# Performance work log

Measured on AMD Instinct MI355X. Metric: run time of the kernel, lower is better.

## Reference

```python
import jax, jax.numpy as jnp
import numpy as np

B, SQ, SK, H = 8, 2048, 2048, 256
NH, HD = 4, 64  # num_heads, head_dim


def setup_inputs() -> dict:
    key = jax.random.key(0)
    ks = jax.random.split(key, 9)
    scale = 0.02
    inp = {
        'query': jax.random.normal(ks[0], (B, SQ, H), jnp.float32),
        'key':   jax.random.normal(ks[1], (B, SK, H), jnp.float32),
        'value': jax.random.normal(ks[2], (B, SK, H), jnp.float32),
        'mask':  jax.random.bernoulli(ks[3], 0.9, (B, SQ, SK)),
        'Wq': jax.random.normal(ks[4], (H, H), jnp.float32) * scale,
        'bq': jnp.zeros((H,), jnp.float32),
        'Wk': jax.random.normal(ks[5], (H, H), jnp.float32) * scale,
        'bk': jnp.zeros((H,), jnp.float32),
        'Wv': jax.random.normal(ks[6], (H, H), jnp.float32) * scale,
        'bv': jnp.zeros((H,), jnp.float32),
        'Wo': jax.random.normal(ks[7], (H, H), jnp.float32) * scale,
        'bo': jnp.zeros((H,), jnp.float32),
    }
    return inp


def reference(query, key, value, mask, Wq, bq, Wk, bk, Wv, bv, Wo, bo):
    b = query.shape[0]
    scale = jnp.asarray(HD, query.dtype) ** -0.5
    # torch Linear: x @ W.T + b; reshape to [B, NH, S, HD]
    Q = (query @ Wq.T + bq).reshape(b, -1, NH, HD).transpose(0, 2, 1, 3)
    K = (key   @ Wk.T + bk).reshape(b, -1, NH, HD).transpose(0, 2, 1, 3)
    V = (value @ Wv.T + bv).reshape(b, -1, NH, HD).transpose(0, 2, 1, 3)
    scores = jnp.einsum('bhqd,bhkd->bhqk', Q, K) * scale  # [B,NH,SQ,SK]
    # mask-fixing: rows with no valid key get key 0 unmasked
    mask_sum = mask.sum(axis=-1)  # [B,SQ]
    mask_fixed = mask.at[:, :, 0].set(jnp.where(mask_sum == 0, True, mask[:, :, 0]))
    scores = jnp.where(mask_fixed[:, None, :, :], scores, jnp.asarray(-1e9, scores.dtype))
    attn = jax.nn.softmax(scores, axis=-1)
    attn = jnp.where(jnp.isnan(attn), jnp.zeros_like(attn), attn)  # NaN fix
    out = jnp.einsum('bhqk,bhkd->bhqd', attn, V)
    out = out.transpose(0, 2, 1, 3).reshape(b, -1, H)
    out = out @ Wo.T + bo
    return out, attn
```

## Files before the change

### kernel.cpp

```cpp
#include <hip/hip_runtime.h>
#include <math.h>

#define Bn  8
#define SQn 2048
#define SKn 2048
#define Hn  256
#define NHn 4
#define HDn 64
#define SCALEF 0.125f

typedef __attribute__((ext_vector_type(4))) float f32x4;
typedef __attribute__((ext_vector_type(8))) short short8;

__device__ __forceinline__ unsigned short f2bf(float f) {
  unsigned u = __builtin_bit_cast(unsigned, f);
  u += 0x7fffu + ((u >> 16) & 1u);
  return (unsigned short)(u >> 16);
}

__device__ __forceinline__ short8 load8f(const float* p) {
  float4 v0 = *(const float4*)p;
  float4 v1 = *(const float4*)(p + 4);
  short8 r;
  r[0] = (short)f2bf(v0.x); r[1] = (short)f2bf(v0.y);
  r[2] = (short)f2bf(v0.z); r[3] = (short)f2bf(v0.w);
  r[4] = (short)f2bf(v1.x); r[5] = (short)f2bf(v1.y);
  r[6] = (short)f2bf(v1.z); r[7] = (short)f2bf(v1.w);
  return r;
}

__device__ __forceinline__ f32x4 mfma16(short8 a, short8 b, f32x4 c) {
  return __builtin_amdgcn_mfma_f32_16x16x32_bf16(a, b, c, 0, 0, 0);
}

__global__ void detect_mask(const unsigned* __restrict__ m, int* __restrict__ flag) {
  if (threadIdx.x == 0) {
    int f = 0;
    for (int i = 0; i < 64; ++i)
      if (m[i] > 1u) f = 1;
    flag[0] = f;
  }
}

__global__ __launch_bounds__(256) void proj_kernel(
    const float* __restrict__ X, const float* __restrict__ W,
    const float* __restrict__ bias, unsigned short* __restrict__ Y, int vtrans)
{
  const int m0 = blockIdx.x * 64;
  const int n0 = blockIdx.y * 64;
  const int wv = threadIdx.x >> 6;
  const int l  = threadIdx.x & 63;
  const int lr = l & 15, lg = l >> 4;
  const int mrow = m0 + wv * 16 + lr;

  f32x4 acc[4];
  #pragma unroll
  for (int t = 0; t < 4; ++t) acc[t] = (f32x4){0.f, 0.f, 0.f, 0.f};

  const float* ap = X + (size_t)mrow * Hn + lg * 8;
  for (int k0 = 0; k0 < Hn; k0 += 32) {
    short8 a = load8f(ap + k0);
    #pragma unroll
    for (int t = 0; t < 4; ++t) {
      short8 bb = load8f(W + (size_t)(n0 + t * 16 + lr) * Hn + k0 + lg * 8);
      acc[t] = mfma16(a, bb, acc[t]);
    }
  }

  #pragma unroll
  for (int t = 0; t < 4; ++t) {
    const int n = n0 + t * 16 + lr;
    const float bv = bias[n];
    const int h = n >> 6, d = n & 63;
    if (!vtrans) {
      #pragma unroll
      for (int r = 0; r < 4; ++r) {
        const int m = m0 + wv * 16 + lg * 4 + r;
        const int bb = m >> 11, s = m & 2047;
        size_t idx = (((size_t)bb * NHn + h) * SQn + s) * HDn + d;
        Y[idx] = f2bf(acc[t][r] + bv);
      }
    } else {
      const int m = m0 + wv * 16 + lg * 4;
      const int bb = m >> 11, s = m & 2047;
      ushort4 pk;
      pk.x = f2bf(acc[t][0] + bv); pk.y = f2bf(acc[t][1] + bv);
      pk.z = f2bf(acc[t][2] + bv); pk.w = f2bf(acc[t][3] + bv);
      size_t idx = (((size_t)bb * NHn + h) * HDn + d) * (size_t)SKn + s;
      *(ushort4*)(Y + idx) = pk;
    }
  }
}

template <typename T>
__device__ __forceinline__ void load_mask_bits(const T* __restrict__ mp, size_t rowbase,
                                               int colbase, int lr, unsigned mb[4]) {
  #pragma unroll
  for (int r = 0; r < 4; ++r) {
    const T* rp = mp + rowbase + (size_t)r * SKn + colbase + lr;
    unsigned bits = 0;
    #pragma unroll
    for (int t = 0; t < 16; ++t) bits |= (rp[t * 16] != 0 ? 1u : 0u) << t;
    mb[r] = bits;
  }
}

__global__ __launch_bounds__(512) void attn_kernel(
    const unsigned short* __restrict__ Qb, const unsigned short* __restrict__ Kb,
    const unsigned short* __restrict__ Vt, const void* __restrict__ maskp,
    const int* __restrict__ flagp, float* __restrict__ attn_out,
    unsigned short* __restrict__ Ob)
{
  __shared__ __align__(16) unsigned short Plds[16 * 2048];
  float* red = (float*)Plds;
  float* gv  = (float*)Plds + 128;

  const int q0 = blockIdx.x * 16;
  const int h = blockIdx.y, b = blockIdx.z;
  const int wv = threadIdx.x >> 6;
  const int l = threadIdx.x & 63;
  const int lr = l & 15, lg = l >> 4;
  const int colbase = wv * 256;
  const size_t bh = (size_t)b * NHn + h;

  const unsigned short* Qh = Qb + bh * SQn * HDn;
  const unsigned short* Kh = Kb + bh * SKn * HDn;
  const unsigned short* Vh = Vt + bh * HDn * SKn;

  short8 qa0 = *(const short8*)(Qh + (q0 + lr) * HDn + lg * 8);
  short8 qa1 = *(const short8*)(Qh + (q0 + lr) * HDn + 32 + lg * 8);

  f32x4 sc[16];
  #pragma unroll
  for (int t = 0; t < 16; ++t) {
    const int c0 = colbase + t * 16;
    short8 b0 = *(const short8*)(Kh + (size_t)(c0 + lr) * HDn + lg * 8);
    short8 b1 = *(const short8*)(Kh + (size_t)(c0 + lr) * HDn + 32 + lg * 8);
    f32x4 z = (f32x4){0.f, 0.f, 0.f, 0.f};
    z = mfma16(qa0, b0, z);
    z = mfma16(qa1, b1, z);
    sc[t] = z;
  }

  unsigned mb[4];
  const int q_base = q0 + lg * 4;
  const size_t mrowbase = ((size_t)b * SQn + q_base) * (size_t)SKn;
  if (*flagp) load_mask_bits((const unsigned char*)maskp, mrowbase, colbase, lr, mb);
  else        load_mask_bits((const int*)maskp,           mrowbase, colbase, lr, mb);

  float rmax[4] = {-INFINITY, -INFINITY, -INFINITY, -INFINITY};
  #pragma unroll
  for (int t = 0; t < 16; ++t)
    #pragma unroll
    for (int r = 0; r < 4; ++r)
      if ((mb[r] >> t) & 1) rmax[r] = fmaxf(rmax[r], sc[t][r] * SCALEF);
  #pragma unroll
  for (int m = 1; m < 16; m <<= 1)
    #pragma unroll
    for (int r = 0; r < 4; ++r)
      rmax[r] = fmaxf(rmax[r], __shfl_xor(rmax[r], m));
  if (lr == 0)
    #pragma unroll
    for (int r = 0; r < 4; ++r) red[wv * 16 + lg * 4 + r] = rmax[r];
  __syncthreads();
  if (threadIdx.x < 16) {
    float m = red[threadIdx.x];
    for (int w = 1; w < 8; ++w) m = fmaxf(m, red[w * 16 + threadIdx.x]);
    gv[threadIdx.x] = m;
  }
  __syncthreads();

  float gmax[4], rsum[4] = {0.f, 0.f, 0.f, 0.f};
  #pragma unroll
  for (int r = 0; r < 4; ++r) gmax[r] = gv[lg * 4 + r];

  #pragma unroll
  for (int t = 0; t < 16; ++t) {
    const int col = colbase + t * 16 + lr;
    #pragma unroll
    for (int r = 0; r < 4; ++r) {
      float p;
      if (gmax[r] == -INFINITY) p = (col == 0) ? 1.0f : 0.0f;
      else p = ((mb[r] >> t) & 1) ? __expf(sc[t][r] * SCALEF - gmax[r]) : 0.0f;
      sc[t][r] = p;
      rsum[r] += p;
    }
  }
  #pragma unroll
  for (int m = 1; m < 16; m <<= 1)
    #pragma unroll
    for (int r = 0; r < 4; ++r) rsum[r] += __shfl_xor(rsum[r], m);
  if (lr == 0)
    #pragma unroll
    for (int r = 0; r < 4; ++r) red[wv * 16 + lg * 4 + r] = rsum[r];
  __syncthreads();
  if (threadIdx.x < 16) {
    float s = 0.f;
    for (int w = 0; w < 8; ++w) s += red[w * 16 + threadIdx.x];
    gv[threadIdx.x] = s;
  }
  __syncthreads();
  float rinv[4];
  #pragma unroll
  for (int r = 0; r < 4; ++r) rinv[r] = 1.0f / gv[lg * 4 + r];
  __syncthreads();

  #pragma unroll
  for (int t = 0; t < 16; ++t) {
    const int col = colbase + t * 16 + lr;
    #pragma unroll
    for (int r = 0; r < 4; ++r) {
      const int row = lg * 4 + r;
      float a = sc[t][r] * rinv[r];
      attn_out[(bh * SQn + q0 + row) * (size_t)SKn + col] = a;
      unsigned byteoff = (unsigned)row * 4096u + (unsigned)col * 2u;
      byteoff ^= ((unsigned)(row & 7) << 4);
      *(unsigned short*)((char*)Plds + byteoff) = f2bf(a);
    }
  }
  __syncthreads();

  f32x4 oacc[4];
  #pragma unroll
  for (int dt = 0; dt < 4; ++dt) oacc[dt] = (f32x4){0.f, 0.f, 0.f, 0.f};
  #pragma unroll
  for (int ks = 0; ks < 8; ++ks) {
    const int ck = colbase + ks * 32;
    unsigned aoff = (unsigned)lr * 4096u + (unsigned)(ck + lg * 8) * 2u;
    aoff ^= ((unsigned)(lr & 7) << 4);
    short8 pa = *(const short8*)((char*)Plds + aoff);
    #pragma unroll
    for (int dt = 0; dt < 4; ++dt) {
      short8 vb = *(const short8*)(Vh + (size_t)(dt * 16 + lr) * SKn + ck + lg * 8);
      oacc[dt] = mfma16(pa, vb, oacc[dt]);
    }
  }
  __syncthreads();

  float* Op = (float*)Plds;
  #pragma unroll
  for (int dt = 0; dt < 4; ++dt)
    #pragma unroll
    for (int r = 0; r < 4; ++r)
      Op[(wv * 16 + lg * 4 + r) * 64 + dt * 16 + lr] = oacc[dt][r];
  __syncthreads();
  for (int e = threadIdx.x; e < 1024; e += 512) {
    const int row = e >> 6, d = e & 63;
    float s = 0.f;
    for (int w = 0; w < 8; ++w) s += Op[w * 1024 + row * 64 + d];
    Ob[((size_t)b * SQn + q0 + row) * Hn + h * HDn + d] = f2bf(s);
  }
}

__global__ __launch_bounds__(256) void oproj_kernel(
    const unsigned short* __restrict__ A, const float* __restrict__ W,
    const float* __restrict__ bias, float* __restrict__ out)
{
  const int m0 = blockIdx.x * 64;
  const int n0 = blockIdx.y * 64;
  const int wv = threadIdx.x >> 6;
  const int l  = threadIdx.x & 63;
  const int lr = l & 15, lg = l >> 4;
  const int mrow = m0 + wv * 16 + lr;

  f32x4 acc[4];
  #pragma unroll
  for (int t = 0; t < 4; ++t) acc[t] = (f32x4){0.f, 0.f, 0.f, 0.f};

  for (int k0 = 0; k0 < Hn; k0 += 32) {
    short8 a = *(const short8*)(A + (size_t)mrow * Hn + k0 + lg * 8);
    #pragma unroll
    for (int t = 0; t < 4; ++t) {
      short8 bb = load8f(W + (size_t)(n0 + t * 16 + lr) * Hn + k0 + lg * 8);
      acc[t] = mfma16(a, bb, acc[t]);
    }
  }
  #pragma unroll
  for (int t = 0; t < 4; ++t) {
    const int n = n0 + t * 16 + lr;
    const float bv = bias[n];
    #pragma unroll
    for (int r = 0; r < 4; ++r) {
      const int m = m0 + wv * 16 + lg * 4 + r;
      out[(size_t)m * Hn + n] = acc[t][r] + bv;
    }
  }
}

extern "C" void kernel_launch(void* const* d_in, const int* in_sizes, int n_in,
                              void* d_out, int out_size, void* d_ws, size_t ws_size,
                              hipStream_t stream) {
  const float* query = (const float*)d_in[0];
  const float* key_  = (const float*)d_in[1];
  const float* value = (const float*)d_in[2];
  const void*  mask  = d_in[3];
  const float* Wq = (const float*)d_in[4];
  const float* bq = (const float*)d_in[5];
  const float* Wk = (const float*)d_in[6];
  const float* bk = (const float*)d_in[7];
  const float* Wv = (const float*)d_in[8];
  const float* bv = (const float*)d_in[9];
  const float* Wo = (const float*)d_in[10];
  const float* bo = (const float*)d_in[11];

  float* out  = (float*)d_out;
  float* attn = out + (size_t)Bn * SQn * Hn;

  char* ws = (char*)d_ws;
  int* flag = (int*)ws;
  unsigned short* Qb = (unsigned short*)(ws + 256);
  unsigned short* Kb = Qb + (size_t)Bn * SQn * Hn;
  unsigned short* Vt = Kb + (size_t)Bn * SKn * Hn;
  unsigned short* Ob = Vt + (size_t)Bn * SKn * Hn;

  detect_mask<<<1, 64, 0, stream>>>((const unsigned*)mask, flag);

  dim3 pg(256, 4);
  proj_kernel<<<pg, 256, 0, stream>>>(query, Wq, bq, Qb, 0);
  proj_kernel<<<pg, 256, 0, stream>>>(key_,  Wk, bk, Kb, 0);
  proj_kernel<<<pg, 256, 0, stream>>>(value, Wv, bv, Vt, 1);

  attn_kernel<<<dim3(SQn / 16, NHn, Bn), 512, 0, stream>>>(
      Qb, Kb, Vt, mask, flag, attn, Ob);

  oproj_kernel<<<dim3(256, 4), 256, 0, stream>>>(Ob, Wo, bo, out);
}
```

Measured before the change: 516.0 us.

## Restructure attention to per-wave two-pass online softmax without LDS or block syncs

The 512-thread block that split the key range across 8 waves and reduced through shared memory is replaced by one wave per 16-row query tile. Each wave runs two passes over all keys: an online max/sum pass, then a pass that recomputes scores, writes normalized attention with vectorized stores and feeds bf16 probabilities straight into the PV MFMAs. The mask is read once with wide loads into a bitmask kept in registers, and blocks are remapped with a swizzle. This removes LDS traffic, block barriers and the cross-wave output reduction, at the cost of computing QK^T twice and holding 16 mask words per lane.

```diff
diff --git a/kernel.cpp b/kernel.cpp
--- a/kernel.cpp
+++ b/kernel.cpp
@@ -8,9 +8,13 @@
 #define NHn 4
 #define HDn 64
 #define SCALEF 0.125f
+#define NEGBIG -1e30f
 
 typedef __attribute__((ext_vector_type(4))) float f32x4;
+typedef __attribute__((ext_vector_type(4))) unsigned int u32x4;
 typedef __attribute__((ext_vector_type(8))) short short8;
+typedef unsigned short ushort_t;
+typedef unsigned long long ull_t;
 
 __device__ __forceinline__ unsigned short f2bf(float f) {
   unsigned u = __builtin_bit_cast(unsigned, f);
@@ -92,164 +96,167 @@
   }
 }
 
-template <typename T>
-__device__ __forceinline__ void load_mask_bits(const T* __restrict__ mp, size_t rowbase,
-                                               int colbase, int lr, unsigned mb[4]) {
-  #pragma unroll
-  for (int r = 0; r < 4; ++r) {
-    const T* rp = mp + rowbase + (size_t)r * SKn + colbase + lr;
-    unsigned bits = 0;
-    #pragma unroll
-    for (int t = 0; t < 16; ++t) bits |= (rp[t * 16] != 0 ? 1u : 0u) << t;
-    mb[r] = bits;
-  }
-}
-
-__global__ __launch_bounds__(512) void attn_kernel(
-    const unsigned short* __restrict__ Qb, const unsigned short* __restrict__ Kb,
-    const unsigned short* __restrict__ Vt, const void* __restrict__ maskp,
-    const int* __restrict__ flagp, float* __restrict__ attn_out,
-    unsigned short* __restrict__ Ob)
+template <int BYTEMASK>
+__device__ __forceinline__ void attn_wave(
+    int rt, const ushort_t* __restrict__ Qb, const ushort_t* __restrict__ Kb,
+    const ushort_t* __restrict__ Vt, const void* __restrict__ maskp,
+    float* __restrict__ attn_out, ushort_t* __restrict__ Ob)
 {
-  __shared__ __align__(16) unsigned short Plds[16 * 2048];
-  float* red = (float*)Plds;
-  float* gv  = (float*)Plds + 128;
-
-  const int q0 = blockIdx.x * 16;
-  const int h = blockIdx.y, b = blockIdx.z;
-  const int wv = threadIdx.x >> 6;
-  const int l = threadIdx.x & 63;
+  const int l  = threadIdx.x & 63;
   const int lr = l & 15, lg = l >> 4;
-  const int colbase = wv * 256;
-  const size_t bh = (size_t)b * NHn + h;
-
-  const unsigned short* Qh = Qb + bh * SQn * HDn;
-  const unsigned short* Kh = Kb + bh * SKn * HDn;
-  const unsigned short* Vh = Vt + bh * HDn * SKn;
+  const int bh = rt >> 7;
+  const int q0 = (rt & 127) << 4;
+  const int b  = bh >> 2, h = bh & 3;
+
+  const ushort_t* Qh = Qb + (size_t)bh * SQn * HDn;
+  const ushort_t* Kh = Kb + (size_t)bh * SKn * HDn;
+  const ushort_t* Vh = Vt + (size_t)bh * HDn * SKn;
 
   short8 qa0 = *(const short8*)(Qh + (q0 + lr) * HDn + lg * 8);
   short8 qa1 = *(const short8*)(Qh + (q0 + lr) * HDn + 32 + lg * 8);
 
-  f32x4 sc[16];
-  #pragma unroll
-  for (int t = 0; t < 16; ++t) {
-    const int c0 = colbase + t * 16;
-    short8 b0 = *(const short8*)(Kh + (size_t)(c0 + lr) * HDn + lg * 8);
-    short8 b1 = *(const short8*)(Kh + (size_t)(c0 + lr) * HDn + 32 + lg * 8);
-    f32x4 z = (f32x4){0.f, 0.f, 0.f, 0.f};
-    z = mfma16(qa0, b0, z);
-    z = mfma16(qa1, b1, z);
-    sc[t] = z;
-  }
-
-  unsigned mb[4];
-  const int q_base = q0 + lg * 4;
-  const size_t mrowbase = ((size_t)b * SQn + q_base) * (size_t)SKn;
-  if (*flagp) load_mask_bits((const unsigned char*)maskp, mrowbase, colbase, lr, mb);
-  else        load_mask_bits((const int*)maskp,           mrowbase, colbase, lr, mb);
-
-  float rmax[4] = {-INFINITY, -INFINITY, -INFINITY, -INFINITY};
-  #pragma unroll
-  for (int t = 0; t < 16; ++t)
+  const int krA = (lr >> 2) * 8 + (lr & 3);
+  const size_t mrowelem = ((size_t)b * SQn + q0 + lr) * (size_t)SKn;
+
+  unsigned mb[16];
+  for (int g = 0; g < 16; ++g) {
+    unsigned word = 0;
+    #pragma unroll
+    for (int s = 0; s < 4; ++s) {
+      const int c = (g * 4 + s) * 32;
+      unsigned bits = 0;
+      if (BYTEMASK) {
+        const ull_t* rp = (const ull_t*)((const unsigned char*)maskp + mrowelem + c + lg * 8);
+        ull_t v = *rp;
+        #pragma unroll
+        for (int j = 0; j < 8; ++j)
+          bits |= (((v >> (8 * j)) & 0xFFull) != 0 ? 1u : 0u) << j;
+      } else {
+        const u32x4* rp = (const u32x4*)((const int*)maskp + mrowelem + c + lg * 8);
+        u32x4 x = rp[0];
+        u32x4 y = rp[1];
+        #pragma unroll
+        for (int j = 0; j < 4; ++j) {
+          bits |= (x[j] != 0 ? 1u : 0u) << j;
+          bits |= (y[j] != 0 ? 1u : 0u) << (4 + j);
+        }
+      }
+      word |= bits << (s * 8);
+    }
+    mb[g] = word;
+  }
+
+  float m = NEGBIG, lsum = 0.f;
+  for (int g = 0; g < 16; ++g) {
+    const unsigned mw = mb[g];
+    #pragma unroll
+    for (int s = 0; s < 4; ++s) {
+      const int c = (g * 4 + s) * 32;
+      const ushort_t* kp = Kh + (size_t)(c + krA) * HDn + lg * 8;
+      short8 ka0 = *(const short8*)(kp);
+      short8 ka1 = *(const short8*)(kp + 32);
+      short8 kb0 = *(const short8*)(kp + 4 * HDn);
+      short8 kb1 = *(const short8*)(kp + 4 * HDn + 32);
+      f32x4 za = (f32x4){0.f, 0.f, 0.f, 0.f}, zb = (f32x4){0.f, 0.f, 0.f, 0.f};
+      za = mfma16(ka0, qa0, za); za = mfma16(ka1, qa1, za);
+      zb = mfma16(kb0, qa0, zb); zb = mfma16(kb1, qa1, zb);
+
+      const unsigned bits = (mw >> (s * 8)) & 0xFFu;
+      float sv[8];
+      #pragma unroll
+      for (int j = 0; j < 4; ++j) {
+        sv[j]     = ((bits >> j) & 1) ? za[j] * SCALEF : NEGBIG;
+        sv[4 + j] = ((bits >> (4 + j)) & 1) ? zb[j] * SCALEF : NEGBIG;
+      }
+      float tm = fmaxf(fmaxf(fmaxf(sv[0], sv[1]), fmaxf(sv[2], sv[3])),
+                       fmaxf(fmaxf(sv[4], sv[5]), fmaxf(sv[6], sv[7])));
+      float nm = fmaxf(m, tm);
+      float acc = 0.f;
+      #pragma unroll
+      for (int j = 0; j < 8; ++j) acc += __expf(sv[j] - nm);
+      lsum = lsum * __expf(m - nm) + acc;
+      m = nm;
+    }
+  }
+
+  #pragma unroll
+  for (int d = 16; d < 64; d <<= 1) {
+    float om = __shfl_xor(m, d);
+    float ol = __shfl_xor(lsum, d);
+    float nm = fmaxf(m, om);
+    lsum = lsum * __expf(m - nm) + ol * __expf(om - nm);
+    m = nm;
+  }
+  const bool rowinf = (m < -1e29f);
+  const float m2   = rowinf ? 0.f : m;
+  const float rinv = rowinf ? 0.f : 1.f / lsum;
+
+  float* arow = attn_out + ((size_t)bh * SQn + q0 + lr) * (size_t)SKn;
+  f32x4 oacc[4];
+  #pragma unroll
+  for (int dt = 0; dt < 4; ++dt) oacc[dt] = (f32x4){0.f, 0.f, 0.f, 0.f};
+
+  for (int g = 0; g < 16; ++g) {
+    const unsigned mw = mb[g];
+    #pragma unroll
+    for (int s = 0; s < 4; ++s) {
+      const int c = (g * 4 + s) * 32;
+      const ushort_t* kp = Kh + (size_t)(c + krA) * HDn + lg * 8;
+      short8 ka0 = *(const short8*)(kp);
+      short8 ka1 = *(const short8*)(kp + 32);
+      short8 kb0 = *(const short8*)(kp + 4 * HDn);
+      short8 kb1 = *(const short8*)(kp + 4 * HDn + 32);
+      f32x4 za = (f32x4){0.f, 0.f, 0.f, 0.f}, zb = (f32x4){0.f, 0.f, 0.f, 0.f};
+      za = mfma16(ka0, qa0, za); za = mfma16(ka1, qa1, za);
+      zb = mfma16(kb0, qa0, zb); zb = mfma16(kb1, qa1, zb);
+
+      const unsigned bits = (mw >> (s * 8)) & 0xFFu;
+      float w[8];
+      #pragma unroll
+      for (int j = 0; j < 4; ++j) {
+        float ea = __expf(za[j] * SCALEF - m2) * rinv;
+        float eb = __expf(zb[j] * SCALEF - m2) * rinv;
+        w[j]     = ((bits >> j) & 1) ? ea : 0.f;
+        w[4 + j] = ((bits >> (4 + j)) & 1) ? eb : 0.f;
+      }
+      if (rowinf && c == 0 && lg == 0) w[0] = 1.f;
+
+      f32x4 wa = (f32x4){w[0], w[1], w[2], w[3]};
+      f32x4 wb = (f32x4){w[4], w[5], w[6], w[7]};
+      *(f32x4*)(arow + c + lg * 8)     = wa;
+      *(f32x4*)(arow + c + lg * 8 + 4) = wb;
+
+      short8 pf;
+      #pragma unroll
+      for (int j = 0; j < 8; ++j) pf[j] = (short)f2bf(w[j]);
+      #pragma unroll
+      for (int dt = 0; dt < 4; ++dt) {
+        short8 vb = *(const short8*)(Vh + (size_t)(dt * 16 + lr) * SKn + c + lg * 8);
+        oacc[dt] = mfma16(pf, vb, oacc[dt]);
+      }
+    }
+  }
+
+  #pragma unroll
+  for (int dt = 0; dt < 4; ++dt)
     #pragma unroll
     for (int r = 0; r < 4; ++r)
-      if ((mb[r] >> t) & 1) rmax[r] = fmaxf(rmax[r], sc[t][r] * SCALEF);
-  #pragma unroll
-  for (int m = 1; m < 16; m <<= 1)
-    #pragma unroll
-    for (int r = 0; r < 4; ++r)
-      rmax[r] = fmaxf(rmax[r], __shfl_xor(rmax[r], m));
-  if (lr == 0)
-    #pragma unroll
-    for (int r = 0; r < 4; ++r) red[wv * 16 + lg * 4 + r] = rmax[r];
-  __syncthreads();
-  if (threadIdx.x < 16) {
-    float m = red[threadIdx.x];
-    for (int w = 1; w < 8; ++w) m = fmaxf(m, red[w * 16 + threadIdx.x]);
-    gv[threadIdx.x] = m;
-  }
-  __syncthreads();
-
-  float gmax[4], rsum[4] = {0.f, 0.f, 0.f, 0.f};
-  #pragma unroll
-  for (int r = 0; r < 4; ++r) gmax[r] = gv[lg * 4 + r];
-
-  #pragma unroll
-  for (int t = 0; t < 16; ++t) {
-    const int col = colbase + t * 16 + lr;
-    #pragma unroll
-    for (int r = 0; r < 4; ++r) {
-      float p;
-      if (gmax[r] == -INFINITY) p = (col == 0) ? 1.0f : 0.0f;
-      else p = ((mb[r] >> t) & 1) ? __expf(sc[t][r] * SCALEF - gmax[r]) : 0.0f;
-      sc[t][r] = p;
-      rsum[r] += p;
-    }
-  }
-  #pragma unroll
-  for (int m = 1; m < 16; m <<= 1)
-    #pragma unroll
-    for (int r = 0; r < 4; ++r) rsum[r] += __shfl_xor(rsum[r], m);
-  if (lr == 0)
-    #pragma unroll
-    for (int r = 0; r < 4; ++r) red[wv * 16 + lg * 4 + r] = rsum[r];
-  __syncthreads();
-  if (threadIdx.x < 16) {
-    float s = 0.f;
-    for (int w = 0; w < 8; ++w) s += red[w * 16 + threadIdx.x];
-    gv[threadIdx.x] = s;
-  }
-  __syncthreads();
-  float rinv[4];
-  #pragma unroll
-  for (int r = 0; r < 4; ++r) rinv[r] = 1.0f / gv[lg * 4 + r];
-  __syncthreads();
-
-  #pragma unroll
-  for (int t = 0; t < 16; ++t) {
-    const int col = colbase + t * 16 + lr;
-    #pragma unroll
-    for (int r = 0; r < 4; ++r) {
-      const int row = lg * 4 + r;
-      float a = sc[t][r] * rinv[r];
-      attn_out[(bh * SQn + q0 + row) * (size_t)SKn + col] = a;
-      unsigned byteoff = (unsigned)row * 4096u + (unsigned)col * 2u;
-      byteoff ^= ((unsigned)(row & 7) << 4);
-      *(unsigned short*)((char*)Plds + byteoff) = f2bf(a);
-    }
-  }
-  __syncthreads();
-
-  f32x4 oacc[4];
-  #pragma unroll
-  for (int dt = 0; dt < 4; ++dt) oacc[dt] = (f32x4){0.f, 0.f, 0.f, 0.f};
-  #pragma unroll
-  for (int ks = 0; ks < 8; ++ks) {
-    const int ck = colbase + ks * 32;
-    unsigned aoff = (unsigned)lr * 4096u + (unsigned)(ck + lg * 8) * 2u;
-    aoff ^= ((unsigned)(lr & 7) << 4);
-    short8 pa = *(const short8*)((char*)Plds + aoff);
-    #pragma unroll
-    for (int dt = 0; dt < 4; ++dt) {
-      short8 vb = *(const short8*)(Vh + (size_t)(dt * 16 + lr) * SKn + ck + lg * 8);
-      oacc[dt] = mfma16(pa, vb, oacc[dt]);
-    }
-  }
-  __syncthreads();
-
-  float* Op = (float*)Plds;
-  #pragma unroll
-  for (int dt = 0; dt < 4; ++dt)
-    #pragma unroll
-    for (int r = 0; r < 4; ++r)
-      Op[(wv * 16 + lg * 4 + r) * 64 + dt * 16 + lr] = oacc[dt][r];
-  __syncthreads();
-  for (int e = threadIdx.x; e < 1024; e += 512) {
-    const int row = e >> 6, d = e & 63;
-    float s = 0.f;
-    for (int w = 0; w < 8; ++w) s += Op[w * 1024 + row * 64 + d];
-    Ob[((size_t)b * SQn + q0 + row) * Hn + h * HDn + d] = f2bf(s);
-  }
+      Ob[((size_t)b * SQn + q0 + lg * 4 + r) * Hn + h * HDn + dt * 16 + lr] =
+          f2bf(oacc[dt][r]);
+}
+
+__global__ __launch_bounds__(256) void attn_kernel(
+    const ushort_t* __restrict__ Qb, const ushort_t* __restrict__ Kb,
+    const ushort_t* __restrict__ Vt, const void* __restrict__ maskp,
+    const int* __restrict__ flagp, float* __restrict__ attn_out,
+    ushort_t* __restrict__ Ob)
+{
+  const int wv = threadIdx.x >> 6;
+  const int bid = blockIdx.x;
+  const int swz = (bid & 7) * 128 + (bid >> 3);
+  const int rt = swz * 4 + wv;
+  if (*flagp) attn_wave<1>(rt, Qb, Kb, Vt, maskp, attn_out, Ob);
+  else        attn_wave<0>(rt, Qb, Kb, Vt, maskp, attn_out, Ob);
 }
 
 __global__ __launch_bounds__(256) void oproj_kernel(
@@ -320,8 +327,7 @@
   proj_kernel<<<pg, 256, 0, stream>>>(key_,  Wk, bk, Kb, 0);
   proj_kernel<<<pg, 256, 0, stream>>>(value, Wv, bv, Vt, 1);
 
-  attn_kernel<<<dim3(SQn / 16, NHn, Bn), 512, 0, stream>>>(
-      Qb, Kb, Vt, mask, flag, attn, Ob);
+  attn_kernel<<<1024, 256, 0, stream>>>(Qb, Kb, Vt, mask, flag, attn, Ob);
 
   oproj_kernel<<<dim3(256, 4), 256, 0, stream>>>(Ob, Wo, bo, out);
 }
```

Result: slower. 760.8 us (+47.4%).
